# Kernel tuning notes

Measured on AMD Instinct MI355X. Metric: run time of the kernel, lower is better.

Reference implementation:

```python
import jax, jax.numpy as jnp
import numpy as np

B, S, H = 32, 4096, 512

def setup_inputs() -> dict:
    key = jax.random.key(0)
    k1, k2, k3, k4, k5 = jax.random.split(key, 5)
    scale = 1.0 / np.sqrt(H)
    return {
        "query": jax.random.normal(k1, (B, 1, H), dtype=jnp.float32),
        "keys": jax.random.normal(k2, (B, S, H), dtype=jnp.float32),
        "Wa": jax.random.normal(k3, (H, H), dtype=jnp.float32) * scale,
        "Ua": jax.random.normal(k4, (H, H), dtype=jnp.float32) * scale,
        "Va": jax.random.normal(k5, (H, 1), dtype=jnp.float32) * scale,
    }

def reference(query, keys, Wa, Ua, Va):
    # additive (Bahdanau) attention scores: Va^T tanh(Wa q + Ua k)
    q_proj = jnp.einsum('bqh,hd->bqd', query, Wa)          # [B,1,H]
    k_proj = jnp.einsum('bsh,hd->bsd', keys, Ua)           # [B,S,H]
    scores = jnp.einsum('bsd,d->bs', jnp.tanh(q_proj + k_proj), Va[:, 0])  # [B,S]
    weights = jax.nn.softmax(scores, axis=-1)[:, None, :]  # [B,1,S]
    context = jnp.einsum('bqs,bsh->bqh', weights, keys)    # [B,1,H]
    return (context, weights)
```

## Files before the change

kernel.cpp:

```cpp
#include <hip/hip_runtime.h>
#include <hip/hip_bf16.h>

#define B_ 32
#define S_ 4096
#define H_ 512

typedef short bf16x8 __attribute__((ext_vector_type(8)));
typedef float f32x4 __attribute__((ext_vector_type(4)));

__device__ inline unsigned short f2bf(float x) {
    unsigned u = __float_as_uint(x);
    return (unsigned short)((u + 0x7fffu + ((u >> 16) & 1u)) >> 16);
}

__device__ __forceinline__ unsigned cvt2(float a, float b) {
    __hip_bfloat162 h = __float22bfloat162_rn(float2{a, b});
    return *reinterpret_cast<unsigned*>(&h);
}

__device__ inline float fast_tanh(float x) {
    float e = __expf(2.f * x);
    return 1.f - 2.f / (e + 1.f);
}

__device__ __forceinline__ void stage16(const void* g, void* lds_base) {
    __builtin_amdgcn_global_load_lds(
        (const __attribute__((address_space(1))) unsigned char*)g,
        (__attribute__((address_space(3))) unsigned char*)lds_base, 16, 0, 0);
}

__global__ void k_prep_ua(const float* __restrict__ Ua,
                          unsigned short* __restrict__ ua_t) {
    __shared__ float tile[32][33];
    int h0 = blockIdx.x * 32, d0 = blockIdx.y * 32;
    int tx = threadIdx.x, ty = threadIdx.y;
#pragma unroll
    for (int j = 0; j < 4; ++j)
        tile[ty + j * 8][tx] = Ua[(size_t)(h0 + ty + j * 8) * H_ + d0 + tx];
    __syncthreads();
#pragma unroll
    for (int j = 0; j < 4; ++j) {
        int dl = ty + j * 8;
        ua_t[(size_t)(d0 + dl) * H_ + h0 + tx] = f2bf(tile[tx][dl]);
    }
}

__global__ __launch_bounds__(512) void k_qproj(const float* __restrict__ query,
                                               const float* __restrict__ Wa,
                                               float* __restrict__ qproj) {
    __shared__ float q[H_];
    int b = blockIdx.x, d = threadIdx.x;
    q[d] = query[(size_t)b * H_ + d];
    __syncthreads();
    float acc = 0.f;
    for (int h = 0; h < H_; ++h)
        acc = fmaf(q[h], Wa[(size_t)h * H_ + d], acc);
    qproj[(size_t)b * H_ + d] = acc;
}

__global__ __launch_bounds__(256, 2) void k_scores(
    const float* __restrict__ keys, const unsigned short* __restrict__ ua_t,
    const float* __restrict__ qproj, const float* __restrict__ Va,
    float* __restrict__ part_sc) {
    __shared__ __align__(16) unsigned char As[2][16384];
    __shared__ __align__(16) unsigned char Bs[2][16384];
    __shared__ float smp[2][128];

    int tid = threadIdx.x;
    int wave = tid >> 6, lane = tid & 63;
    int lq = lane & 15, lh = lane >> 4;
    int wm = wave >> 1, wn = wave & 1;

    int logical = (blockIdx.x & 7) * 512 + (blockIdx.x >> 3);
    int b  = logical >> 7;
    int m0 = ((logical >> 2) & 31) * 128;
    int nb = logical & 3;

    const float* keysb = keys + (size_t)b * S_ * H_;

    int arow_t = tid >> 4;
    int acolf  = (tid & 15) * 4;
    const float* aptr = keysb + (size_t)(m0 + arow_t) * H_ + acolf;
    unsigned awb = (unsigned)(arow_t * 128 + (((tid & 15) * 8) ^ ((arow_t & 7) << 4)));

    int rbl = lane >> 3;
    unsigned cbb = (unsigned)(((lane & 7) * 16) ^ (rbl << 4));
    const unsigned char* uab = (const unsigned char*)ua_t;
    const unsigned char* bsrc[4];
    unsigned bdst[4];
#pragma unroll
    for (int i = 0; i < 4; ++i) {
        int j = wave * 4 + i;
        bsrc[i] = uab + ((size_t)(nb * 128 + 8 * j + rbl)) * 1024 + cbb;
        bdst[i] = (unsigned)(j * 1024);
    }

    f32x4 acc[4][4];
#pragma unroll
    for (int i = 0; i < 4; ++i)
#pragma unroll
        for (int j = 0; j < 4; ++j) acc[i][j] = (f32x4){0.f, 0.f, 0.f, 0.f};

#pragma unroll
    for (int i = 0; i < 4; ++i) stage16(bsrc[i], &Bs[0][bdst[i]]);
    {
        float4 a0[8];
#pragma unroll
        for (int j = 0; j < 8; ++j)
            a0[j] = *(const float4*)(aptr + (size_t)j * 16 * H_);
#pragma unroll
        for (int j = 0; j < 8; ++j) {
            uint2 w;
            w.x = cvt2(a0[j].x, a0[j].y);
            w.y = cvt2(a0[j].z, a0[j].w);
            *(uint2*)(&As[0][0] + awb + j * 2048) = w;
        }
    }
    __syncthreads();

#pragma unroll
    for (int t = 0; t < 8; ++t) {
        const int cur = t & 1, nxt = cur ^ 1;
        float4 ar[8];
        if (t < 7) {
#pragma unroll
            for (int i = 0; i < 4; ++i)
                stage16(bsrc[i] + (t + 1) * 128, &Bs[nxt][bdst[i]]);
#pragma unroll
            for (int j = 0; j < 8; ++j)
                ar[j] = *(const float4*)(aptr + (size_t)j * 16 * H_ + (t + 1) * 64);
        }
#pragma unroll
        for (int ks = 0; ks < 2; ++ks) {
            bf16x8 af[4], bv[4];
            unsigned koff = (unsigned)(ks * 64 + lh * 16);
#pragma unroll
            for (int mf = 0; mf < 4; ++mf) {
                unsigned R = (unsigned)(wm * 64 + mf * 16 + lq);
                af[mf] = *(const bf16x8*)(&As[cur][0] + R * 128 + (koff ^ ((R & 7) << 4)));
            }
#pragma unroll
            for (int nf = 0; nf < 4; ++nf) {
                unsigned R = (unsigned)(wn * 64 + nf * 16 + lq);
                bv[nf] = *(const bf16x8*)(&Bs[cur][0] + R * 128 + (koff ^ ((R & 7) << 4)));
            }
#pragma unroll
            for (int mf = 0; mf < 4; ++mf)
#pragma unroll
                for (int nf = 0; nf < 4; ++nf)
                    acc[mf][nf] = __builtin_amdgcn_mfma_f32_16x16x32_bf16(
                        af[mf], bv[nf], acc[mf][nf], 0, 0, 0);
        }
        if (t < 7) {
#pragma unroll
            for (int j = 0; j < 8; ++j) {
                uint2 w;
                w.x = cvt2(ar[j].x, ar[j].y);
                w.y = cvt2(ar[j].z, ar[j].w);
                *(uint2*)(&As[nxt][0] + awb + j * 2048) = w;
            }
        }
        __syncthreads();
    }

    float va_r[4], qp_r[4];
#pragma unroll
    for (int nf = 0; nf < 4; ++nf) {
        int n = nb * 128 + wn * 64 + nf * 16 + lq;
        va_r[nf] = Va[n];
        qp_r[nf] = qproj[(size_t)b * H_ + n];
    }
#pragma unroll
    for (int mf = 0; mf < 4; ++mf) {
#pragma unroll
        for (int reg = 0; reg < 4; ++reg) {
            float p = 0.f;
#pragma unroll
            for (int nf = 0; nf < 4; ++nf)
                p += va_r[nf] * fast_tanh(qp_r[nf] + acc[mf][nf][reg]);
            p += __shfl_xor(p, 1);
            p += __shfl_xor(p, 2);
            p += __shfl_xor(p, 4);
            p += __shfl_xor(p, 8);
            if (lq == 0) smp[wn][wm * 64 + mf * 16 + lh * 4 + reg] = p;
        }
    }
    __syncthreads();
    if (tid < 128) {
        float s = smp[0][tid] + smp[1][tid];
        part_sc[((size_t)nb * B_ + b) * S_ + m0 + tid] = s;
    }
}

__global__ __launch_bounds__(512) void k_softmax(const float* __restrict__ part_sc,
                                                 float* __restrict__ wts) {
    __shared__ float red[8];
    int b = blockIdx.x, tid = threadIdx.x;
    const float* p0 = part_sc + (size_t)b * S_;
    const float* p1 = p0 + (size_t)B_ * S_;
    const float* p2 = p1 + (size_t)B_ * S_;
    const float* p3 = p2 + (size_t)B_ * S_;
    float v[8];
    float m = -1e30f;
#pragma unroll
    for (int i = 0; i < 8; ++i) {
        int s = tid + i * 512;
        v[i] = ((p0[s] + p1[s]) + (p2[s] + p3[s]));
        m = fmaxf(m, v[i]);
    }
#pragma unroll
    for (int o = 1; o < 64; o <<= 1) m = fmaxf(m, __shfl_xor(m, o));
    if ((tid & 63) == 0) red[tid >> 6] = m;
    __syncthreads();
    m = red[0];
#pragma unroll
    for (int w = 1; w < 8; ++w) m = fmaxf(m, red[w]);
    float sum = 0.f;
#pragma unroll
    for (int i = 0; i < 8; ++i) {
        v[i] = __expf(v[i] - m);
        sum += v[i];
    }
#pragma unroll
    for (int o = 1; o < 64; o <<= 1) sum += __shfl_xor(sum, o);
    __syncthreads();
    if ((tid & 63) == 0) red[tid >> 6] = sum;
    __syncthreads();
    float tot = 0.f;
#pragma unroll
    for (int w = 0; w < 8; ++w) tot += red[w];
    float inv = 1.f / tot;
#pragma unroll
    for (int i = 0; i < 8; ++i) wts[(size_t)b * S_ + tid + i * 512] = v[i] * inv;
}

__global__ __launch_bounds__(512) void k_ctx_part(const float* __restrict__ keys,
                                                  const float* __restrict__ wts,
                                                  float* __restrict__ part) {
    int c = blockIdx.x, b = blockIdx.y, h = threadIdx.x;
    const float* wrow = wts + (size_t)b * S_ + c * 128;
    const float* kbase = keys + ((size_t)b * S_ + c * 128) * H_ + h;
    float acc = 0.f;
#pragma unroll 8
    for (int s = 0; s < 128; ++s)
        acc = fmaf(wrow[s], kbase[(size_t)s * H_], acc);
    part[((size_t)c * B_ + b) * H_ + h] = acc;
}

__global__ __launch_bounds__(512) void k_ctx_reduce(const float* __restrict__ part,
                                                    float* __restrict__ ctx) {
    int b = blockIdx.x, h = threadIdx.x;
    float s = 0.f;
#pragma unroll
    for (int c = 0; c < 32; ++c) s += part[((size_t)c * B_ + b) * H_ + h];
    ctx[(size_t)b * H_ + h] = s;
}

extern "C" void kernel_launch(void* const* d_in, const int* in_sizes, int n_in,
                              void* d_out, int out_size, void* d_ws, size_t ws_size,
                              hipStream_t stream) {
    const float* query = (const float*)d_in[0];
    const float* keys  = (const float*)d_in[1];
    const float* Wa    = (const float*)d_in[2];
    const float* Ua    = (const float*)d_in[3];
    const float* Va    = (const float*)d_in[4];

    float* out = (float*)d_out;
    float* ctx = out;
    float* wts = out + B_ * H_;

    char* ws = (char*)d_ws;
    unsigned short* ua_t = (unsigned short*)ws;
    float* qproj   = (float*)(ws + 524288);
    float* part_sc = (float*)(ws + 524288 + 65536);
    float* part_cx = (float*)(ws + 524288 + 65536 + 2097152);

    k_prep_ua<<<dim3(16, 16), dim3(32, 8), 0, stream>>>(Ua, ua_t);
    k_qproj<<<dim3(32), dim3(512), 0, stream>>>(query, Wa, qproj);
    k_scores<<<dim3(4096), dim3(256), 0, stream>>>(keys, ua_t, qproj, Va, part_sc);
    k_softmax<<<dim3(32), dim3(512), 0, stream>>>(part_sc, wts);
    k_ctx_part<<<dim3(32, 32), dim3(512), 0, stream>>>(keys, wts, part_cx);
    k_ctx_reduce<<<dim3(32), dim3(512), 0, stream>>>(part_cx, ctx);
}
```

Measured before the change: 216.5 us.

## Prefetch keys tile two steps ahead with register double-buffering and manual waitcnt

The A-operand (keys, fp32 to bf16) global loads now run two k-steps ahead using two register buffers. The LDS write for the next tile happens before the MFMA block instead of after it. __syncthreads is replaced with explicit s_waitcnt vmcnt(8)/lgkmcnt(0) plus s_barrier and sched_barrier, so one batch of global loads stays in flight across the barrier. The aim is to hide global memory latency better, at the cost of more VGPRs and fragile hand-counted wait values.

```diff
diff --git a/kernel.cpp b/kernel.cpp
--- a/kernel.cpp
+++ b/kernel.cpp
@@ -79,8 +79,7 @@
     const float* keysb = keys + (size_t)b * S_ * H_;
 
     int arow_t = tid >> 4;
-    int acolf  = (tid & 15) * 4;
-    const float* aptr = keysb + (size_t)(m0 + arow_t) * H_ + acolf;
+    const float* aptr = keysb + (size_t)(m0 + arow_t) * H_ + (tid & 15) * 4;
     unsigned awb = (unsigned)(arow_t * 128 + (((tid & 15) * 8) ^ ((arow_t & 7) << 4)));
 
     int rbl = lane >> 3;
@@ -101,34 +100,46 @@
 #pragma unroll
         for (int j = 0; j < 4; ++j) acc[i][j] = (f32x4){0.f, 0.f, 0.f, 0.f};
 
-#pragma unroll
-    for (int i = 0; i < 4; ++i) stage16(bsrc[i], &Bs[0][bdst[i]]);
-    {
-        float4 a0[8];
+    float4 arA[8], arB[8];
+
+    auto loadA = [&](float4 (&arr)[8], int tt) {
 #pragma unroll
         for (int j = 0; j < 8; ++j)
-            a0[j] = *(const float4*)(aptr + (size_t)j * 16 * H_);
+            arr[j] = *(const float4*)(aptr + (size_t)j * 16 * H_ + tt * 64);
+    };
+    auto writeA = [&](const float4 (&arr)[8], int buf) {
 #pragma unroll
         for (int j = 0; j < 8; ++j) {
             uint2 w;
-            w.x = cvt2(a0[j].x, a0[j].y);
-            w.y = cvt2(a0[j].z, a0[j].w);
-            *(uint2*)(&As[0][0] + awb + j * 2048) = w;
-        }
-    }
-    __syncthreads();
+            w.x = cvt2(arr[j].x, arr[j].y);
+            w.y = cvt2(arr[j].z, arr[j].w);
+            *(uint2*)(&As[buf][0] + awb + j * 2048) = w;
+        }
+    };
+
+#pragma unroll
+    for (int i = 0; i < 4; ++i) stage16(bsrc[i], &Bs[0][bdst[i]]);
+    loadA(arA, 0);
+    loadA(arB, 1);
+    writeA(arA, 0);
+    asm volatile("s_waitcnt lgkmcnt(0)" ::: "memory");
+    __builtin_amdgcn_s_barrier();
+    __builtin_amdgcn_sched_barrier(0);
 
 #pragma unroll
     for (int t = 0; t < 8; ++t) {
         const int cur = t & 1, nxt = cur ^ 1;
-        float4 ar[8];
         if (t < 7) {
 #pragma unroll
             for (int i = 0; i < 4; ++i)
                 stage16(bsrc[i] + (t + 1) * 128, &Bs[nxt][bdst[i]]);
-#pragma unroll
-            for (int j = 0; j < 8; ++j)
-                ar[j] = *(const float4*)(aptr + (size_t)j * 16 * H_ + (t + 1) * 64);
+        }
+        if (t < 6) {
+            if ((t & 1) == 0) loadA(arA, t + 2); else loadA(arB, t + 2);
+        }
+        __builtin_amdgcn_sched_barrier(0);
+        if (t < 7) {
+            if ((t & 1) == 0) writeA(arB, nxt); else writeA(arA, nxt);
         }
 #pragma unroll
         for (int ks = 0; ks < 2; ++ks) {
@@ -151,16 +162,13 @@
                     acc[mf][nf] = __builtin_amdgcn_mfma_f32_16x16x32_bf16(
                         af[mf], bv[nf], acc[mf][nf], 0, 0, 0);
         }
-        if (t < 7) {
-#pragma unroll
-            for (int j = 0; j < 8; ++j) {
-                uint2 w;
-                w.x = cvt2(ar[j].x, ar[j].y);
-                w.y = cvt2(ar[j].z, ar[j].w);
-                *(uint2*)(&As[nxt][0] + awb + j * 2048) = w;
-            }
-        }
-        __syncthreads();
+        if (t < 6) {
+            asm volatile("s_waitcnt vmcnt(8) lgkmcnt(0)" ::: "memory");
+        } else {
+            asm volatile("s_waitcnt vmcnt(0) lgkmcnt(0)" ::: "memory");
+        }
+        __builtin_amdgcn_s_barrier();
+        __builtin_amdgcn_sched_barrier(0);
     }
 
     float va_r[4], qp_r[4];
```

Measured after the change: 217.5 us. Within noise of the previous version (+0.4%).
